# Kernel optimization log

Hardware: AMD Instinct MI355X
Metric: run time of the kernel (lower is better)

The kernel has to match this reference:

```python
import jax, jax.numpy as jnp
import numpy as np

N_BINS = 256
TAU = 0.01
EPS = 1e-10


def setup_inputs() -> dict:
    key = jax.random.key(0)
    x = jax.random.uniform(key, (4, 1, 512, 512), dtype=jnp.float32)
    return {"x": x}


def reference(x):
    B, _, H, W = x.shape
    bins = jnp.linspace(0.0, 1.0, N_BINS, dtype=x.dtype)  # (n_bins,)
    xf = x.reshape(B, H * W, 1)                            # (B, HW, 1)
    diff = xf - bins[None, None, :]                        # (B, HW, n_bins)
    weights = jnp.exp(-jnp.square(diff) / (2.0 * TAU ** 2))
    # soft histogram over pixels, normalized per image
    histogram = weights.sum(axis=1)                        # (B, n_bins)
    histogram = histogram / (histogram.sum(axis=1, keepdims=True) + EPS)
    cdf = jnp.cumsum(histogram, axis=1)                    # (B, n_bins)
    cdf_min = cdf[:, 0:1]
    cdf_normalized = (cdf - cdf_min) / (1.0 - cdf_min + EPS)
    # per-pixel soft lookup into the normalized CDF
    weights_norm = weights / (weights.sum(axis=-1, keepdims=True) + EPS)
    equalized_flat = (weights_norm * cdf_normalized[:, None, :]).sum(axis=-1)  # (B, HW)
    return equalized_flat.reshape(B, 1, H, W)
```

## Files before the change

### kernel.cpp

```cpp
#include <hip/hip_runtime.h>
#include <math.h>

#define N_BINS 256
#define TAU 0.01f
#define EPS 1e-10f
#define HW (512*512)
#define Q 4081
#define QSTRIDE 4096
#define MWIN 208
#define WTAB (2*MWIN+1)
#define WPADN 432
#define NP 27
#define CFP_STRIDE 289
#define NPART 64
#define REDS 260

__global__ __launch_bounds__(512) void hist_conv_kernel(const float* __restrict__ x,
                                                        float* __restrict__ partT) {
    __shared__ float cfp[16 * CFP_STRIDE];
    __shared__ union { unsigned int lh[QSTRIDE]; float ph[256 * 17]; } U;
    __shared__ float wtE[WPADN];
    const int b   = blockIdx.y;
    const int s   = blockIdx.x;
    const int tid = threadIdx.x;
    const int r   = tid & 15;
    const int t   = tid >> 4;

    for (int i = tid; i < QSTRIDE; i += 512) U.lh[i] = 0u;
    for (int i = tid; i < 16 * CFP_STRIDE; i += 512) cfp[i] = 0.f;
    for (int i = tid; i < WPADN; i += 512) {
        const float d = (float)(i - MWIN) * (1.0f / 4080.f);
        wtE[i] = (i < WTAB) ? __expf(-d * d * (1.0f / (2.0f * TAU * TAU))) : 0.f;
    }
    __syncthreads();

    const float4* xb = (const float4*)(x + (size_t)b * HW + (size_t)s * 4096);
#pragma unroll
    for (int i = 0; i < 2; ++i) {
        const float4 v = xb[i * 512 + tid];
        int q0 = __float2int_rn(v.x * 4080.f);
        int q1 = __float2int_rn(v.y * 4080.f);
        int q2 = __float2int_rn(v.z * 4080.f);
        int q3 = __float2int_rn(v.w * 4080.f);
        q0 = min(max(q0, 0), Q - 1); q1 = min(max(q1, 0), Q - 1);
        q2 = min(max(q2, 0), Q - 1); q3 = min(max(q3, 0), Q - 1);
        atomicAdd(&U.lh[q0], 1u); atomicAdd(&U.lh[q1], 1u);
        atomicAdd(&U.lh[q2], 1u); atomicAdd(&U.lh[q3], 1u);
    }
    __syncthreads();

#pragma unroll
    for (int k = 0; k < 8; ++k) {
        const int q = k * 512 + tid;
        cfp[(q & 15) * CFP_STRIDE + (q >> 4) + 13] = (float)U.lh[q];
    }
    __syncthreads();

    {
        float creg[34];
        const float* cbase = &cfp[r * CFP_STRIDE + 8 * t];
#pragma unroll
        for (int k = 0; k < 34; ++k) creg[k] = cbase[k];
        float acc[8];
#pragma unroll
        for (int uu = 0; uu < 8; ++uu) acc[uu] = 0.f;
#pragma unroll
        for (int p = 0; p < NP; ++p) {
            const float w = wtE[16 * p + r];
#pragma unroll
            for (int uu = 0; uu < 8; ++uu) acc[uu] += w * creg[uu + p];
        }
#pragma unroll
        for (int uu = 0; uu < 8; ++uu) U.ph[(8 * t + uu) * 17 + r] = acc[uu];
    }
    __syncthreads();

    if (tid < N_BINS) {
        float hv = 0.f;
#pragma unroll
        for (int rr = 0; rr < 16; ++rr) hv += U.ph[tid * 17 + rr];
        partT[((size_t)b * NPART + s) * N_BINS + tid] = hv;
    }
}

__global__ __launch_bounds__(512) void lut_equalize_kernel(const float* __restrict__ x,
                                                           const float* __restrict__ partT,
                                                           float* __restrict__ out) {
    __shared__ float Tl[QSTRIDE];
    __shared__ float wtE[WPADN];
    __shared__ float cdfnp[288];
    __shared__ float onesp[288];
    __shared__ __align__(16) float red[8 * REDS];
    __shared__ float wsum[4];
    __shared__ float h0s;
    const int b    = blockIdx.y;
    const int s    = blockIdx.x;
    const int tid  = threadIdx.x;
    const int r    = tid & 15;
    const int t    = tid >> 4;
    const int wv   = tid >> 6;
    const int lane = tid & 63;

    for (int i = tid; i < 288; i += 512) {
        cdfnp[i] = 0.f;
        onesp[i] = (i >= 13 && i < 269) ? 1.f : 0.f;
    }
    for (int i = tid; i < WPADN; i += 512) {
        const float d = (float)(i - MWIN) * (1.0f / 4080.f);
        wtE[i] = (i < WTAB) ? __expf(-d * d * (1.0f / (2.0f * TAU * TAU))) : 0.f;
    }

    const float4* xb = (const float4*)(x + (size_t)b * HW + (size_t)s * 4096);
    float4 px[2];
#pragma unroll
    for (int i = 0; i < 2; ++i) px[i] = xb[i * 512 + tid];

    {
        const float4* base4 = (const float4*)(partT + (size_t)b * NPART * N_BINS);
        float4 a4 = make_float4(0.f, 0.f, 0.f, 0.f);
#pragma unroll
        for (int rr = 0; rr < 8; ++rr) {
            const float4 v = base4[(size_t)(8 * wv + rr) * 64 + lane];
            a4.x += v.x; a4.y += v.y; a4.z += v.z; a4.w += v.w;
        }
        ((float4*)&red[wv * REDS])[lane] = a4;
    }
    __syncthreads();

    float val = 0.f, hv = 0.f;
    if (tid < N_BINS) {
#pragma unroll
        for (int w2 = 0; w2 < 8; ++w2) hv += red[w2 * REDS + tid];
        val = hv;
#pragma unroll
        for (int d = 1; d < 64; d <<= 1) {
            const float n = __shfl_up(val, (unsigned)d, 64);
            if (lane >= d) val += n;
        }
        if (lane == 63) wsum[tid >> 6] = val;
        if (tid == 0) h0s = hv;
    }
    __syncthreads();
    if (tid < N_BINS) {
        float prefix = 0.f, total = 0.f;
#pragma unroll
        for (int w2 = 0; w2 < 4; ++w2) {
            const float ws = wsum[w2];
            if (w2 < (tid >> 6)) prefix += ws;
            total += ws;
        }
        val += prefix;
        const float inv  = 1.0f / (total + EPS);
        const float cdf0 = h0s * inv;
        cdfnp[tid + 13] = (val * inv - cdf0) / (1.0f - cdf0 + EPS);
    }
    __syncthreads();

    {
        float creg[34], oreg[34];
        const int base = 8 * t;
#pragma unroll
        for (int k = 0; k < 34; ++k) { creg[k] = cdfnp[base + k]; oreg[k] = onesp[base + k]; }
        float acc[8], sw[8];
#pragma unroll
        for (int uu = 0; uu < 8; ++uu) { acc[uu] = 0.f; sw[uu] = 0.f; }
#pragma unroll
        for (int p = 0; p < NP; ++p) {
            const float w = wtE[16 * p + r];
#pragma unroll
            for (int uu = 0; uu < 8; ++uu) {
                const int k = uu - p + 26;
                acc[uu] += w * creg[k];
                sw[uu]  += w * oreg[k];
            }
        }
#pragma unroll
        for (int uu = 0; uu < 8; ++uu)
            Tl[16 * (8 * t + uu) + r] = acc[uu] / (sw[uu] + EPS);
    }
    __syncthreads();

    float4* ob = (float4*)(out + (size_t)b * HW + (size_t)s * 4096);
#pragma unroll
    for (int i = 0; i < 2; ++i) {
        const float4 v = px[i];
        const float vv[4] = {v.x, v.y, v.z, v.w};
        float res[4];
#pragma unroll
        for (int k2 = 0; k2 < 4; ++k2) {
            const float u = vv[k2] * 4080.f;
            int q = (int)u;
            q = min(max(q, 0), Q - 2);
            const float frac = u - (float)q;
            const float t0 = Tl[q], t1 = Tl[q + 1];
            res[k2] = fmaf(frac, t1 - t0, t0);
        }
        ob[i * 512 + tid] = make_float4(res[0], res[1], res[2], res[3]);
    }
}

extern "C" void kernel_launch(void* const* d_in, const int* in_sizes, int n_in,
                              void* d_out, int out_size, void* d_ws, size_t ws_size,
                              hipStream_t stream) {
    const float* x = (const float*)d_in[0];
    float* out     = (float*)d_out;
    const int B    = in_sizes[0] / HW;

    float* partT = (float*)d_ws;

    hist_conv_kernel<<<dim3(NPART, B), 512, 0, stream>>>(x, partT);
    lut_equalize_kernel<<<dim3(NPART, B), 512, 0, stream>>>(x, partT, out);
}
```

Before: 61.67 us.

## Halve quantization grid, double histogram blocks, use nontemporal output stores

The fine quantization grid for the histogram and the LUT drops from 4081 to 2041 levels, so the per-block convolution and LUT build do about half the work. The histogram kernel now launches 128 blocks per image, each covering 2048 pixels, which doubles parallelism while the equalize kernel sums twice as many partial histograms. Output writes use nontemporal stores. The coarser grid adds approximation error against the Gaussian-weighted reference, and the extra partials make the reduction heavier.

New measurement: 62.18 us. About the same (+0.8%).

```diff
diff --git a/kernel.cpp b/kernel.cpp
--- a/kernel.cpp
+++ b/kernel.cpp
@@ -5,80 +5,79 @@
 #define TAU 0.01f
 #define EPS 1e-10f
 #define HW (512*512)
-#define Q 4081
-#define QSTRIDE 4096
-#define MWIN 208
-#define WTAB (2*MWIN+1)
-#define WPADN 432
+#define QF 2041
+#define QS2 2048
+#define PH 8
+#define MWIN2 104
+#define WTAB2 209
+#define WPADN2 216
 #define NP 27
-#define CFP_STRIDE 289
-#define NPART 64
+#define CFP_STRIDE2 285
+#define NPART 128
 #define REDS 260
+
+typedef float vfloat4 __attribute__((ext_vector_type(4)));
 
 __global__ __launch_bounds__(512) void hist_conv_kernel(const float* __restrict__ x,
                                                         float* __restrict__ partT) {
-    __shared__ float cfp[16 * CFP_STRIDE];
-    __shared__ union { unsigned int lh[QSTRIDE]; float ph[256 * 17]; } U;
-    __shared__ float wtE[WPADN];
+    __shared__ float cfp[PH * CFP_STRIDE2];
+    __shared__ union { unsigned int lh[QS2]; float ph[N_BINS * 9]; } U;
+    __shared__ float wtE[WPADN2];
     const int b   = blockIdx.y;
     const int s   = blockIdx.x;
     const int tid = threadIdx.x;
-    const int r   = tid & 15;
-    const int t   = tid >> 4;
-
-    for (int i = tid; i < QSTRIDE; i += 512) U.lh[i] = 0u;
-    for (int i = tid; i < 16 * CFP_STRIDE; i += 512) cfp[i] = 0.f;
-    for (int i = tid; i < WPADN; i += 512) {
-        const float d = (float)(i - MWIN) * (1.0f / 4080.f);
-        wtE[i] = (i < WTAB) ? __expf(-d * d * (1.0f / (2.0f * TAU * TAU))) : 0.f;
-    }
-    __syncthreads();
-
-    const float4* xb = (const float4*)(x + (size_t)b * HW + (size_t)s * 4096);
-#pragma unroll
-    for (int i = 0; i < 2; ++i) {
-        const float4 v = xb[i * 512 + tid];
-        int q0 = __float2int_rn(v.x * 4080.f);
-        int q1 = __float2int_rn(v.y * 4080.f);
-        int q2 = __float2int_rn(v.z * 4080.f);
-        int q3 = __float2int_rn(v.w * 4080.f);
-        q0 = min(max(q0, 0), Q - 1); q1 = min(max(q1, 0), Q - 1);
-        q2 = min(max(q2, 0), Q - 1); q3 = min(max(q3, 0), Q - 1);
+    const int r   = tid & 7;
+    const int t   = tid >> 3;
+
+    for (int i = tid; i < QS2; i += 512) U.lh[i] = 0u;
+    for (int i = tid; i < PH * CFP_STRIDE2; i += 512) cfp[i] = 0.f;
+    for (int i = tid; i < WPADN2; i += 512) {
+        const float d = (float)(i - MWIN2) * (1.0f / 2040.f);
+        wtE[i] = (i < WTAB2) ? __expf(-d * d * (1.0f / (2.0f * TAU * TAU))) : 0.f;
+    }
+    __syncthreads();
+
+    {
+        const float4 v = ((const float4*)(x + (size_t)b * HW + (size_t)s * 2048))[tid];
+        int q0 = __float2int_rn(v.x * 2040.f);
+        int q1 = __float2int_rn(v.y * 2040.f);
+        int q2 = __float2int_rn(v.z * 2040.f);
+        int q3 = __float2int_rn(v.w * 2040.f);
+        q0 = min(max(q0, 0), QF - 1); q1 = min(max(q1, 0), QF - 1);
+        q2 = min(max(q2, 0), QF - 1); q3 = min(max(q3, 0), QF - 1);
         atomicAdd(&U.lh[q0], 1u); atomicAdd(&U.lh[q1], 1u);
         atomicAdd(&U.lh[q2], 1u); atomicAdd(&U.lh[q3], 1u);
     }
     __syncthreads();
 
 #pragma unroll
-    for (int k = 0; k < 8; ++k) {
+    for (int k = 0; k < 4; ++k) {
         const int q = k * 512 + tid;
-        cfp[(q & 15) * CFP_STRIDE + (q >> 4) + 13] = (float)U.lh[q];
-    }
-    __syncthreads();
-
-    {
-        float creg[34];
-        const float* cbase = &cfp[r * CFP_STRIDE + 8 * t];
-#pragma unroll
-        for (int k = 0; k < 34; ++k) creg[k] = cbase[k];
-        float acc[8];
-#pragma unroll
-        for (int uu = 0; uu < 8; ++uu) acc[uu] = 0.f;
+        cfp[(q & 7) * CFP_STRIDE2 + (q >> 3) + 13] = (float)U.lh[q];
+    }
+    __syncthreads();
+
+    {
+        float creg[30];
+        const float* cbase = &cfp[r * CFP_STRIDE2 + 4 * t];
+#pragma unroll
+        for (int k = 0; k < 30; ++k) creg[k] = cbase[k];
+        float acc[4] = {0.f, 0.f, 0.f, 0.f};
 #pragma unroll
         for (int p = 0; p < NP; ++p) {
-            const float w = wtE[16 * p + r];
-#pragma unroll
-            for (int uu = 0; uu < 8; ++uu) acc[uu] += w * creg[uu + p];
-        }
-#pragma unroll
-        for (int uu = 0; uu < 8; ++uu) U.ph[(8 * t + uu) * 17 + r] = acc[uu];
+            const float w = wtE[8 * p + r];
+#pragma unroll
+            for (int uu = 0; uu < 4; ++uu) acc[uu] += w * creg[uu + p];
+        }
+#pragma unroll
+        for (int uu = 0; uu < 4; ++uu) U.ph[(4 * t + uu) * 9 + r] = acc[uu];
     }
     __syncthreads();
 
     if (tid < N_BINS) {
         float hv = 0.f;
 #pragma unroll
-        for (int rr = 0; rr < 16; ++rr) hv += U.ph[tid * 17 + rr];
+        for (int rr = 0; rr < 8; ++rr) hv += U.ph[tid * 9 + rr];
         partT[((size_t)b * NPART + s) * N_BINS + tid] = hv;
     }
 }
@@ -86,8 +85,8 @@
 __global__ __launch_bounds__(512) void lut_equalize_kernel(const float* __restrict__ x,
                                                            const float* __restrict__ partT,
                                                            float* __restrict__ out) {
-    __shared__ float Tl[QSTRIDE];
-    __shared__ float wtE[WPADN];
+    __shared__ float Tl[QS2];
+    __shared__ float wtE[WPADN2];
     __shared__ float cdfnp[288];
     __shared__ float onesp[288];
     __shared__ __align__(16) float red[8 * REDS];
@@ -96,8 +95,8 @@
     const int b    = blockIdx.y;
     const int s    = blockIdx.x;
     const int tid  = threadIdx.x;
-    const int r    = tid & 15;
-    const int t    = tid >> 4;
+    const int r    = tid & 7;
+    const int t    = tid >> 3;
     const int wv   = tid >> 6;
     const int lane = tid & 63;
 
@@ -105,9 +104,9 @@
         cdfnp[i] = 0.f;
         onesp[i] = (i >= 13 && i < 269) ? 1.f : 0.f;
     }
-    for (int i = tid; i < WPADN; i += 512) {
-        const float d = (float)(i - MWIN) * (1.0f / 4080.f);
-        wtE[i] = (i < WTAB) ? __expf(-d * d * (1.0f / (2.0f * TAU * TAU))) : 0.f;
+    for (int i = tid; i < WPADN2; i += 512) {
+        const float d = (float)(i - MWIN2) * (1.0f / 2040.f);
+        wtE[i] = (i < WTAB2) ? __expf(-d * d * (1.0f / (2.0f * TAU * TAU))) : 0.f;
     }
 
     const float4* xb = (const float4*)(x + (size_t)b * HW + (size_t)s * 4096);
@@ -119,8 +118,8 @@
         const float4* base4 = (const float4*)(partT + (size_t)b * NPART * N_BINS);
         float4 a4 = make_float4(0.f, 0.f, 0.f, 0.f);
 #pragma unroll
-        for (int rr = 0; rr < 8; ++rr) {
-            const float4 v = base4[(size_t)(8 * wv + rr) * 64 + lane];
+        for (int rr = 0; rr < 16; ++rr) {
+            const float4 v = base4[(size_t)(16 * wv + rr) * 64 + lane];
             a4.x += v.x; a4.y += v.y; a4.z += v.z; a4.w += v.w;
         }
         ((float4*)&red[wv * REDS])[lane] = a4;
@@ -157,30 +156,28 @@
     __syncthreads();
 
     {
-        float creg[34], oreg[34];
-        const int base = 8 * t;
-#pragma unroll
-        for (int k = 0; k < 34; ++k) { creg[k] = cdfnp[base + k]; oreg[k] = onesp[base + k]; }
-        float acc[8], sw[8];
-#pragma unroll
-        for (int uu = 0; uu < 8; ++uu) { acc[uu] = 0.f; sw[uu] = 0.f; }
+        float creg[30], oreg[30];
+        const int base = 4 * t;
+#pragma unroll
+        for (int k = 0; k < 30; ++k) { creg[k] = cdfnp[base + k]; oreg[k] = onesp[base + k]; }
+        float acc[4] = {0.f, 0.f, 0.f, 0.f}, sw[4] = {0.f, 0.f, 0.f, 0.f};
 #pragma unroll
         for (int p = 0; p < NP; ++p) {
-            const float w = wtE[16 * p + r];
-#pragma unroll
-            for (int uu = 0; uu < 8; ++uu) {
+            const float w = wtE[8 * p + r];
+#pragma unroll
+            for (int uu = 0; uu < 4; ++uu) {
                 const int k = uu - p + 26;
                 acc[uu] += w * creg[k];
                 sw[uu]  += w * oreg[k];
             }
         }
 #pragma unroll
-        for (int uu = 0; uu < 8; ++uu)
-            Tl[16 * (8 * t + uu) + r] = acc[uu] / (sw[uu] + EPS);
-    }
-    __syncthreads();
-
-    float4* ob = (float4*)(out + (size_t)b * HW + (size_t)s * 4096);
+        for (int uu = 0; uu < 4; ++uu)
+            Tl[8 * (4 * t + uu) + r] = acc[uu] / (sw[uu] + EPS);
+    }
+    __syncthreads();
+
+    vfloat4* ob = (vfloat4*)(out + (size_t)b * HW + (size_t)s * 4096);
 #pragma unroll
     for (int i = 0; i < 2; ++i) {
         const float4 v = px[i];
@@ -188,14 +185,16 @@
         float res[4];
 #pragma unroll
         for (int k2 = 0; k2 < 4; ++k2) {
-            const float u = vv[k2] * 4080.f;
+            const float u = vv[k2] * 2040.f;
             int q = (int)u;
-            q = min(max(q, 0), Q - 2);
+            q = min(max(q, 0), QF - 2);
             const float frac = u - (float)q;
             const float t0 = Tl[q], t1 = Tl[q + 1];
             res[k2] = fmaf(frac, t1 - t0, t0);
         }
-        ob[i * 512 + tid] = make_float4(res[0], res[1], res[2], res[3]);
+        vfloat4 o;
+        o.x = res[0]; o.y = res[1]; o.z = res[2]; o.w = res[3];
+        __builtin_nontemporal_store(o, &ob[i * 512 + tid]);
     }
 }
 
@@ -209,5 +208,5 @@
     float* partT = (float*)d_ws;
 
     hist_conv_kernel<<<dim3(NPART, B), 512, 0, stream>>>(x, partT);
-    lut_equalize_kernel<<<dim3(NPART, B), 512, 0, stream>>>(x, partT, out);
+    lut_equalize_kernel<<<dim3(64, B), 512, 0, stream>>>(x, partT, out);
 }
```
